# Kernel tuning notes

Measured on AMD Instinct MI355X. Metric: run time of the kernel, lower is better.

Reference implementation:

```python
import jax, jax.numpy as jnp
import numpy as np
from jax import lax

WS = 8
NH = 16

def _conv1x1(t, w):
    # w: (Cout, Cin), t: (B,C,H,W)
    return jnp.einsum('oc,bchw->bohw', w, t)

def _bn(t, g, b, m, v, eps=1e-5):
    s = g * lax.rsqrt(v + eps)
    return (t - m[:, None, None]) * s[:, None, None] + b[:, None, None]

def _forward(x, qkv_w, l2_w, bn2_g, bn2_b, bn2_m, bn2_v, wq, wk, wv, rel_x, rel_y,
             l1_bias, rel_table, dw_w, bnp_g, bnp_b, bnp_m, bnp_v, pw_w):
    B, C, H, W = x.shape
    ws, nh = WS, NH
    d = C // nh
    scale = d ** -0.5

    # ---- local2: 1x1 conv + BN (inference) ----
    local = _bn(_conv1x1(x, l2_w), bn2_g, bn2_b, bn2_m, bn2_v)

    # ---- local1: SelfAttentionConv2d, k=3, pad=1, groups=1 ----
    xp = jnp.pad(x, ((0, 0), (0, 0), (1, 1), (1, 1)))  # zero pad
    vq = _conv1x1(xp, wq)
    vk = _conv1x1(xp, wk)
    vv = _conv1x1(xp, wv)
    win_q = vq[:, :, 1:H + 1, 1:W + 1]  # center crop -> (B,C,H,W)
    def patches3(t):
        p = jnp.stack([t[:, :, i:i + H, j:j + W] for i in range(3) for j in range(3)], axis=-1)
        return p.reshape(B, C, H, W, 3, 3)
    pk = patches3(vk)
    pv = patches3(vv)
    rs = C // 2
    qx = jnp.einsum('bxhw,xk->bhwk', win_q[:, :rs], rel_x)  # (B,H,W,3)
    qy = jnp.einsum('byhw,yk->bhwk', win_q[:, rs:], rel_y)
    logits = jnp.einsum('bchw,bchwkl->bhwkl', win_q, pk)
    logits = logits + qx[:, :, :, None, :] + qy[:, :, :, :, None]
    a = jax.nn.softmax(logits.reshape(B, H, W, 9), axis=-1).reshape(B, H, W, 3, 3)
    local = local + jnp.einsum('bhwkl,bchwkl->bchw', a, pv) + l1_bias[None, :, None, None]

    # ---- windowed MHSA (H, W divisible by ws so pad() is a no-op) ----
    qkv = _conv1x1(x, qkv_w)  # (B, 3C, H, W)
    hh, ww = H // ws, W // ws
    t = qkv.reshape(B, 3, nh, d, hh, ws, ww, ws)
    t = t.transpose(1, 0, 4, 6, 2, 5, 7, 3).reshape(3, B * hh * ww, nh, ws * ws, d)
    q, k, v = t[0], t[1], t[2]
    dots = jnp.einsum('wnid,wnjd->wnij', q, k) * scale
    # relative position bias
    coords = np.stack(np.meshgrid(np.arange(ws), np.arange(ws), indexing='ij')).reshape(2, -1)
    rel = (coords[:, :, None] - coords[:, None, :]).transpose(1, 2, 0) + (ws - 1)
    idx = rel[..., 0] * (2 * ws - 1) + rel[..., 1]  # (ws*ws, ws*ws)
    rpb = rel_table[idx.reshape(-1)].reshape(ws * ws, ws * ws, nh).transpose(2, 0, 1)
    dots = dots + rpb[None]
    attn = jnp.einsum('wnij,wnjd->wnid', jax.nn.softmax(dots, axis=-1), v)
    attn = attn.reshape(B, hh, ww, nh, ws, ws, d).transpose(0, 3, 6, 1, 4, 2, 5).reshape(B, C, H, W)

    # ---- pooling edge-correction branches ----
    pad_h = jnp.pad(attn, ((0, 0), (0, 0), (0, 1), (0, 0)), mode='reflect')
    pad_w = jnp.pad(attn, ((0, 0), (0, 0), (0, 0), (0, 1)), mode='reflect')
    p = ws // 2 - 1
    mph = lax.reduce_window(pad_h, -jnp.inf, lax.max, (1, 1, ws, 1), (1, 1, 1, 1),
                            [(0, 0), (0, 0), (p, p), (0, 0)])
    mpw = lax.reduce_window(pad_w, -jnp.inf, lax.max, (1, 1, 1, ws), (1, 1, 1, 1),
                            [(0, 0), (0, 0), (0, 0), (p, p)])
    aph = lax.reduce_window(pad_h, 0.0, lax.add, (1, 1, ws, 1), (1, 1, 1, 1),
                            [(0, 0), (0, 0), (p, p), (0, 0)]) / ws
    apw = lax.reduce_window(pad_w, 0.0, lax.add, (1, 1, 1, ws), (1, 1, 1, 1),
                            [(0, 0), (0, 0), (0, 0), (p, p)]) / ws
    out = mph + mpw + aph + apw + local

    # ---- proj: reflect pad_out + depthwise 8x8 conv (pad 3) + BN + 1x1 ----
    out = jnp.pad(out, ((0, 0), (0, 0), (0, 1), (0, 1)), mode='reflect')
    out = lax.conv_general_dilated(out, dw_w, (1, 1), [(3, 3), (3, 3)],
                                   dimension_numbers=('NCHW', 'OIHW', 'NCHW'),
                                   feature_group_count=C)
    out = _bn(out, bnp_g, bnp_b, bnp_m, bnp_v)
    out = _conv1x1(out, pw_w)
    return out[:, :, :H, :W]


def setup_inputs() -> dict:
    key = jax.random.key(0)
    ks = jax.random.split(key, 20)
    C = 256
    n = lambda k, shp, s=1.0: jax.random.normal(k, shp, dtype=jnp.float32) * s
    u = lambda k, shp: jax.random.uniform(k, shp, dtype=jnp.float32, minval=0.5, maxval=1.5)
    fan = 1.0 / 16.0  # 1/sqrt(256)
    return {
        'x': n(ks[0], (2, C, 96, 96)),
        'qkv_w': n(ks[1], (3 * C, C), fan),
        'l2_w': n(ks[2], (C, C), fan),
        'bn2_g': u(ks[3], (C,)), 'bn2_b': n(ks[4], (C,), 0.1),
        'bn2_m': n(ks[5], (C,), 0.1), 'bn2_v': u(ks[6], (C,)),
        'wq': n(ks[7], (C, C), fan), 'wk': n(ks[8], (C, C), fan), 'wv': n(ks[9], (C, C), fan),
        'rel_x': n(ks[10], (C // 2, 3), 0.1), 'rel_y': n(ks[11], (C // 2, 3), 0.1),
        'l1_bias': n(ks[12], (C,), 0.05),
        'rel_table': n(ks[13], (15 * 15, NH), 0.02),
        'dw_w': n(ks[14], (C, 1, 8, 8), 1.0 / 8.0),
        'bnp_g': u(ks[15], (C,)), 'bnp_b': n(ks[16], (C,), 0.1),
        'bnp_m': n(ks[17], (C,), 0.1), 'bnp_v': u(ks[18], (C,)),
        'pw_w': n(ks[19], (C, C), fan),
    }


def reference(x, qkv_w, l2_w, bn2_g, bn2_b, bn2_m, bn2_v, wq, wk, wv, rel_x, rel_y,
              l1_bias, rel_table, dw_w, bnp_g, bnp_b, bnp_m, bnp_v, pw_w):
    return _forward(x, qkv_w, l2_w, bn2_g, bn2_b, bn2_m, bn2_v, wq, wk, wv, rel_x, rel_y,
                    l1_bias, rel_table, dw_w, bnp_g, bnp_b, bnp_m, bnp_v, pw_w)
```

## Files before the change

kernel.cpp:

```cpp
#include <hip/hip_runtime.h>
#include <math.h>


namespace {

constexpr int NP = 96 * 96;
constexpr int C  = 256;

typedef __bf16 bf16x8 __attribute__((ext_vector_type(8)));
typedef __bf16 bf16x4 __attribute__((ext_vector_type(4)));
typedef float  f32x4  __attribute__((ext_vector_type(4)));
typedef float  f32x16 __attribute__((ext_vector_type(16)));

__device__ __forceinline__ unsigned short f2bf_rne(float f) {
  unsigned u = __float_as_uint(f);
  u += 0x7FFFu + ((u >> 16) & 1u);
  return (unsigned short)(u >> 16);
}
__device__ __forceinline__ __bf16 f2bf16(float f) {
  unsigned short s = f2bf_rne(f);
  return *(__bf16*)&s;
}
__device__ __forceinline__ float bf2f(unsigned short s) {
  unsigned u = (unsigned)s << 16;
  return __uint_as_float(u);
}
__device__ __forceinline__ float4 bf4_to_f4(const unsigned short* p) {
  bf16x4 v = *(const bf16x4*)p;
  float4 r;
  r.x = (float)v[0]; r.y = (float)v[1]; r.z = (float)v[2]; r.w = (float)v[3];
  return r;
}

__global__ __launch_bounds__(256) void prep(
    const float* __restrict__ x,
    const float* __restrict__ l2, const float* __restrict__ q,
    const float* __restrict__ k,  const float* __restrict__ v,
    const float* __restrict__ qkv, const float* __restrict__ pw,
    unsigned short* __restrict__ XT, unsigned short* __restrict__ W7)
{
  __shared__ float tile[64][65];
  const int bx = blockIdx.x;
  const int t = threadIdx.x;
  if (bx < 2048) {
    const int row = bx;
    const float* src; int r;
    if      (row <  256) { src = l2;  r = row; }
    else if (row <  512) { src = q;   r = row - 256; }
    else if (row <  768) { src = k;   r = row - 512; }
    else if (row < 1024) { src = v;   r = row - 768; }
    else if (row < 1792) { src = qkv; r = row - 1024; }
    else                 { src = pw;  r = row - 1792; }
    W7[row * 256 + t] = f2bf_rne(src[r * 256 + t]);
    return;
  }
  const int xb = bx - 2048;
  const int p0 = (xb % 144) * 64;
  const int c0 = ((xb / 144) % 4) * 64;
  const int b  = xb / 576;
  const float* xb_p = x + (long)b * C * NP;
#pragma unroll
  for (int i = 0; i < 4; ++i) {
    int s = i * 256 + t;
    int c = s >> 4, p4 = s & 15;
    float4 vv = *(const float4*)&xb_p[(long)(c0 + c) * NP + p0 + p4 * 4];
    tile[c][p4 * 4 + 0] = vv.x;
    tile[c][p4 * 4 + 1] = vv.y;
    tile[c][p4 * 4 + 2] = vv.z;
    tile[c][p4 * 4 + 3] = vv.w;
  }
  __syncthreads();
  unsigned short* XTb = XT + (long)b * NP * 256;
#pragma unroll
  for (int i = 0; i < 2; ++i) {
    int s = i * 256 + t;
    int p = s >> 3, c8 = s & 7;
    unsigned short u[8];
#pragma unroll
    for (int e = 0; e < 8; ++e) u[e] = f2bf_rne(tile[c8 * 8 + e][p]);
    *(uint4*)&XTb[(long)(p0 + p) * 256 + c0 + c8 * 8] = *(const uint4*)u;
  }
}

__global__ __launch_bounds__(256) void xpose(
    const float* __restrict__ x, unsigned short* __restrict__ XT)
{
  __shared__ float tile[64][65];
  const int t = threadIdx.x;
  const int p0 = blockIdx.x * 64, c0 = blockIdx.y * 64, b = blockIdx.z;
  const float* xb = x + (long)b * C * NP;
#pragma unroll
  for (int i = 0; i < 4; ++i) {
    int s = i * 256 + t;
    int c = s >> 4, p4 = s & 15;
    float4 v = *(const float4*)&xb[(long)(c0 + c) * NP + p0 + p4 * 4];
    tile[c][p4 * 4 + 0] = v.x;
    tile[c][p4 * 4 + 1] = v.y;
    tile[c][p4 * 4 + 2] = v.z;
    tile[c][p4 * 4 + 3] = v.w;
  }
  __syncthreads();
  unsigned short* XTb = XT + (long)b * NP * 256;
#pragma unroll
  for (int i = 0; i < 2; ++i) {
    int s = i * 256 + t;
    int p = s >> 3, c8 = s & 7;
    unsigned short u[8];
#pragma unroll
    for (int e = 0; e < 8; ++e) u[e] = f2bf_rne(tile[c8 * 8 + e][p]);
    *(uint4*)&XTb[(long)(p0 + p) * 256 + c0 + c8 * 8] = *(const uint4*)u;
  }
}

__global__ __launch_bounds__(256) void gemm_bt(
    const unsigned short* __restrict__ W, const unsigned short* __restrict__ XT,
    unsigned short* __restrict__ O, int Mstride)
{
  __shared__ __align__(16) char smem[36864];
  unsigned short (*As)[40] = reinterpret_cast<unsigned short(*)[40]>(smem);
  unsigned short (*Bs)[40] = reinterpret_cast<unsigned short(*)[40]>(smem + 10240);

  const int t = threadIdx.x;
  const int lane = t & 63, wid = t >> 6;
  const int wm = wid >> 1, wn = wid & 1;
  const int l15 = lane & 15, l4 = lane >> 4;
  const int n0 = blockIdx.x * 128, m0 = blockIdx.y * 128;
  const unsigned short* XTb = XT + (long)blockIdx.z * NP * 256;
  unsigned short* Ob = O + (long)blockIdx.z * NP * Mstride;

  f32x4 acc[4][4];
#pragma unroll
  for (int i = 0; i < 4; ++i)
#pragma unroll
    for (int j = 0; j < 4; ++j) acc[i][j] = (f32x4){0.f, 0.f, 0.f, 0.f};

  for (int k0 = 0; k0 < 256; k0 += 32) {
#pragma unroll
    for (int i = 0; i < 2; ++i) {
      int s = i * 256 + t, r = s >> 2, kc = s & 3;
      *(uint4*)&As[r][kc * 8] =
          *(const uint4*)&W[(long)(m0 + r) * 256 + k0 + kc * 8];
    }
#pragma unroll
    for (int i = 0; i < 2; ++i) {
      int s = i * 256 + t, r = s >> 2, kc = s & 3;
      *(uint4*)&Bs[r][kc * 8] =
          *(const uint4*)&XTb[(long)(n0 + r) * 256 + k0 + kc * 8];
    }
    __syncthreads();

    bf16x8 af[4], bb[4];
#pragma unroll
    for (int mf = 0; mf < 4; ++mf)
      af[mf] = *(const bf16x8*)&As[wm * 64 + mf * 16 + l15][l4 * 8];
#pragma unroll
    for (int nf = 0; nf < 4; ++nf)
      bb[nf] = *(const bf16x8*)&Bs[wn * 64 + nf * 16 + l15][l4 * 8];
#pragma unroll
    for (int mf = 0; mf < 4; ++mf)
#pragma unroll
      for (int nf = 0; nf < 4; ++nf)
        acc[mf][nf] = __builtin_amdgcn_mfma_f32_16x16x32_bf16(
            af[mf], bb[nf], acc[mf][nf], 0, 0, 0);
    __syncthreads();
  }

  unsigned short* trw = (unsigned short*)smem + wid * 64 * 72;
#pragma unroll
  for (int mf = 0; mf < 4; ++mf)
#pragma unroll
    for (int nf = 0; nf < 4; ++nf) {
      unsigned u0 = (unsigned)f2bf_rne(acc[mf][nf][0]) |
                    ((unsigned)f2bf_rne(acc[mf][nf][1]) << 16);
      unsigned u1 = (unsigned)f2bf_rne(acc[mf][nf][2]) |
                    ((unsigned)f2bf_rne(acc[mf][nf][3]) << 16);
      uint2 uu; uu.x = u0; uu.y = u1;
      *(uint2*)&trw[(nf * 16 + l15) * 72 + mf * 16 + l4 * 4] = uu;
    }
  __syncthreads();

  const long pix = n0 + wn * 64 + lane;
  const long rowbase = pix * Mstride + m0 + wm * 64;
#pragma unroll
  for (int cc = 0; cc < 8; ++cc)
    *(uint4*)&Ob[rowbase + cc * 8] = *(const uint4*)&trw[lane * 72 + cc * 8];
}

__global__ __launch_bounds__(256) void gemm_cf32(
    const unsigned short* __restrict__ W, const unsigned short* __restrict__ XT,
    float* __restrict__ Co)
{
  __shared__ unsigned short As[64][40];
  __shared__ unsigned short Bs[128][40];

  const int t = threadIdx.x;
  const int lane = t & 63, wid = t >> 6;
  const int wm = wid >> 1, wn = wid & 1;
  const int l15 = lane & 15, l4 = lane >> 4;
  const int n0 = blockIdx.x * 128, m0 = blockIdx.y * 64;
  const unsigned short* XTb = XT + (long)blockIdx.z * NP * 256;
  float* Cb = Co + (long)blockIdx.z * C * NP;

  f32x4 acc[2][4];
#pragma unroll
  for (int i = 0; i < 2; ++i)
#pragma unroll
    for (int j = 0; j < 4; ++j) acc[i][j] = (f32x4){0.f, 0.f, 0.f, 0.f};

  for (int k0 = 0; k0 < 256; k0 += 32) {
    {
      int r = t >> 2, kc = t & 3;
      *(uint4*)&As[r][kc * 8] =
          *(const uint4*)&W[(long)(m0 + r) * 256 + k0 + kc * 8];
    }
#pragma unroll
    for (int i = 0; i < 2; ++i) {
      int s = i * 256 + t, r = s >> 2, kc = s & 3;
      *(uint4*)&Bs[r][kc * 8] =
          *(const uint4*)&XTb[(long)(n0 + r) * 256 + k0 + kc * 8];
    }
    __syncthreads();

    bf16x8 af[2], bb[4];
#pragma unroll
    for (int mf = 0; mf < 2; ++mf)
      af[mf] = *(const bf16x8*)&As[wm * 32 + mf * 16 + l15][l4 * 8];
#pragma unroll
    for (int nf = 0; nf < 4; ++nf)
      bb[nf] = *(const bf16x8*)&Bs[wn * 64 + nf * 16 + l15][l4 * 8];
#pragma unroll
    for (int mf = 0; mf < 2; ++mf)
#pragma unroll
      for (int nf = 0; nf < 4; ++nf)
        acc[mf][nf] = __builtin_amdgcn_mfma_f32_16x16x32_bf16(
            af[mf], bb[nf], acc[mf][nf], 0, 0, 0);
    __syncthreads();
  }

#pragma unroll
  for (int mf = 0; mf < 2; ++mf)
#pragma unroll
    for (int r = 0; r < 4; ++r) {
      int row = m0 + wm * 32 + mf * 16 + l4 * 4 + r;
#pragma unroll
      for (int nf = 0; nf < 4; ++nf) {
        int col = n0 + wn * 64 + nf * 16 + l15;
        Cb[(long)row * NP + col] = acc[mf][nf][r];
      }
    }
}

__global__ __launch_bounds__(256) void local_attn2(
    const unsigned short* __restrict__ GA,
    const float* __restrict__ rel_x, const float* __restrict__ rel_y,
    const float* __restrict__ bn2_g, const float* __restrict__ bn2_b,
    const float* __restrict__ bn2_m, const float* __restrict__ bn2_v,
    const float* __restrict__ l1_bias, unsigned short* __restrict__ localO)
{
  const int b = blockIdx.y, t = threadIdx.x;
  const int px = t & 31, ch = t >> 5;
  const int p = blockIdx.x * 32 + px;
  const unsigned short* Gb = GA + (long)b * NP * 1024;

  __shared__ float red[8][32][13];
  __shared__ float srel[256 * 3];
  __shared__ float sS[256], sO[256], sBias[256];

  if (t < 128) {
    srel[t * 3 + 0] = rel_x[t * 3 + 0];
    srel[t * 3 + 1] = rel_x[t * 3 + 1];
    srel[t * 3 + 2] = rel_x[t * 3 + 2];
  } else {
    int r = t - 128;
    srel[t * 3 + 0] = rel_y[r * 3 + 0];
    srel[t * 3 + 1] = rel_y[r * 3 + 1];
    srel[t * 3 + 2] = rel_y[r * 3 + 2];
  }
  {
    float s = bn2_g[t] * rsqrtf(bn2_v[t] + 1e-5f);
    sS[t] = s;
    sO[t] = bn2_b[t] - bn2_m[t] * s;
    sBias[t] = l1_bias[t];
  }

  const int h = p / 96, w = p % 96;
  int nof[9];
  float msk[9];
#pragma unroll
  for (int ky = 0; ky < 3; ++ky)
#pragma unroll
    for (int kx = 0; kx < 3; ++kx) {
      int j = ky * 3 + kx, hn = h + ky - 1, wn = w + kx - 1;
      bool v = (hn >= 0 && hn < 96 && wn >= 0 && wn < 96);
      nof[j] = v ? hn * 96 + wn : p;
      msk[j] = v ? 1.f : 0.f;
    }
  __syncthreads();

  float lg[9] = {0, 0, 0, 0, 0, 0, 0, 0, 0};
  float rq[3] = {0, 0, 0};
  const int c0 = ch * 32;
#pragma unroll
  for (int i = 0; i < 4; ++i) {
    const int c = c0 + i * 8;
    bf16x8 q8 = *(const bf16x8*)&Gb[(long)p * 1024 + 256 + c];
    float qv[8];
#pragma unroll
    for (int e = 0; e < 8; ++e) qv[e] = (float)q8[e];
#pragma unroll
    for (int j = 0; j < 9; ++j) {
      bf16x8 k8 = *(const bf16x8*)&Gb[(long)nof[j] * 1024 + 512 + c];
#pragma unroll
      for (int e = 0; e < 8; ++e) lg[j] += qv[e] * (float)k8[e];
    }
#pragma unroll
    for (int e = 0; e < 8; ++e) {
      const float* sr = &srel[(c + e) * 3];
      rq[0] += qv[e] * sr[0];
      rq[1] += qv[e] * sr[1];
      rq[2] += qv[e] * sr[2];
    }
  }
#pragma unroll
  for (int j = 0; j < 9; ++j) red[ch][px][j] = lg[j] * msk[j];
#pragma unroll
  for (int l = 0; l < 3; ++l) red[ch][px][9 + l] = rq[l];
  __syncthreads();

  float a[9];
  float mx = -1e30f;
#pragma unroll
  for (int j = 0; j < 9; ++j) {
    float v = 0.f;
#pragma unroll
    for (int u = 0; u < 8; ++u) v += red[u][px][j];
    float qxl = red[0][px][9 + j % 3] + red[1][px][9 + j % 3] +
                red[2][px][9 + j % 3] + red[3][px][9 + j % 3];
    float qyk = red[4][px][9 + j / 3] + red[5][px][9 + j / 3] +
                red[6][px][9 + j / 3] + red[7][px][9 + j / 3];
    a[j] = v + qxl + qyk;
    mx = fmaxf(mx, a[j]);
  }
  float sum = 0.f;
#pragma unroll
  for (int j = 0; j < 9; ++j) { a[j] = __expf(a[j] - mx); sum += a[j]; }
  const float inv = 1.f / sum;
  float am[9];
#pragma unroll
  for (int j = 0; j < 9; ++j) am[j] = a[j] * inv * msk[j];

#pragma unroll
  for (int i = 0; i < 4; ++i) {
    const int c = c0 + i * 8;
    bf16x8 l28 = *(const bf16x8*)&Gb[(long)p * 1024 + 0 + c];
    float o8[8] = {0, 0, 0, 0, 0, 0, 0, 0};
#pragma unroll
    for (int j = 0; j < 9; ++j) {
      bf16x8 v8 = *(const bf16x8*)&Gb[(long)nof[j] * 1024 + 768 + c];
#pragma unroll
      for (int e = 0; e < 8; ++e) o8[e] += am[j] * (float)v8[e];
    }
#pragma unroll
    for (int e = 0; e < 8; ++e) {
      const int cg = c + e;
      localO[((long)b * C + cg) * NP + p] = f2bf_rne(
          (float)l28[e] * sS[cg] + sO[cg] + o8[e] + sBias[cg]);
    }
  }
}

__global__ __launch_bounds__(64) void window_attn_mfma(
    const unsigned short* __restrict__ QKV,
    const float* __restrict__ rel_table, unsigned short* __restrict__ attnO)
{
  const int win = blockIdx.x, hd = blockIdx.y, b = blockIdx.z;
  const int wy = win / 12, wx = win % 12;
  const int lane = threadIdx.x;
  const int l15 = lane & 15, hi4 = lane >> 4;
  const int l31 = lane & 31, hi2 = lane >> 5;

  __shared__ float srpb[225];
  __shared__ __bf16 P[64][72];

  for (int i = lane; i < 225; i += 64) srpb[i] = rel_table[i * 16 + hd];

  const __bf16* base = (const __bf16*)QKV + (long)b * 9216 * 768;
  const int pixbase = (wy * 8) * 96 + wx * 8;

#define WPIX(i) (pixbase + ((i) >> 3) * 96 + ((i) & 7))

  bf16x8 kf[2], qf[2];
#pragma unroll
  for (int kt = 0; kt < 2; ++kt)
    kf[kt] = *(const bf16x8*)&base[(long)WPIX(32 * kt + l31) * 768 + 256 +
                                   hd * 16 + hi2 * 8];
#pragma unroll
  for (int qt = 0; qt < 2; ++qt)
    qf[qt] = *(const bf16x8*)&base[(long)WPIX(32 * qt + l31) * 768 +
                                   hd * 16 + hi2 * 8];

  bf16x8 vf[2];
#pragma unroll
  for (int kc = 0; kc < 2; ++kc)
#pragma unroll
    for (int j = 0; j < 8; ++j)
      vf[kc][j] = base[(long)WPIX(32 * kc + 8 * hi4 + j) * 768 + 512 +
                       hd * 16 + l15];

  f32x16 S[2][2];
#pragma unroll
  for (int kt = 0; kt < 2; ++kt)
#pragma unroll
    for (int qt = 0; qt < 2; ++qt)
#pragma unroll
      for (int r = 0; r < 16; ++r) S[kt][qt][r] = 0.f;

#pragma unroll
  for (int kt = 0; kt < 2; ++kt)
#pragma unroll
    for (int qt = 0; qt < 2; ++qt)
      S[kt][qt] = __builtin_amdgcn_mfma_f32_32x32x16_bf16(
          kf[kt], qf[qt], S[kt][qt], 0, 0, 0);

  __syncthreads();

  float mx[2] = {-1e30f, -1e30f};
#pragma unroll
  for (int kt = 0; kt < 2; ++kt)
#pragma unroll
    for (int r = 0; r < 16; ++r) {
      const int key = 32 * kt + (r & 3) + 8 * (r >> 2) + 4 * hi2;
      const int ky = key >> 3, kx = key & 7;
#pragma unroll
      for (int qt = 0; qt < 2; ++qt) {
        const int q = 32 * qt + l31;
        const int qy = q >> 3, qx = q & 7;
        float s = S[kt][qt][r] * 0.25f + srpb[(qy - ky + 7) * 15 + (qx - kx + 7)];
        S[kt][qt][r] = s;
        mx[qt] = fmaxf(mx[qt], s);
      }
    }
#pragma unroll
  for (int qt = 0; qt < 2; ++qt)
    mx[qt] = fmaxf(mx[qt], __shfl_xor(mx[qt], 32));

  float sum[2] = {0.f, 0.f};
#pragma unroll
  for (int kt = 0; kt < 2; ++kt)
#pragma unroll
    for (int qt = 0; qt < 2; ++qt)
#pragma unroll
      for (int r = 0; r < 16; ++r) {
        float e = __expf(S[kt][qt][r] - mx[qt]);
        S[kt][qt][r] = e;
        sum[qt] += e;
      }
#pragma unroll
  for (int qt = 0; qt < 2; ++qt) sum[qt] += __shfl_xor(sum[qt], 32);
  const float inv0 = 1.f / sum[0], inv1 = 1.f / sum[1];

#pragma unroll
  for (int qt = 0; qt < 2; ++qt) {
    const float inv = qt ? inv1 : inv0;
#pragma unroll
    for (int kt = 0; kt < 2; ++kt)
#pragma unroll
      for (int rq = 0; rq < 4; ++rq) {
        bf16x4 pk;
#pragma unroll
        for (int j = 0; j < 4; ++j) pk[j] = f2bf16(S[kt][qt][rq * 4 + j] * inv);
        *(bf16x4*)&P[32 * qt + l31][32 * kt + 8 * rq + 4 * hi2] = pk;
      }
  }
  __syncthreads();

  f32x4 o[4];
#pragma unroll
  for (int qt4 = 0; qt4 < 4; ++qt4) o[qt4] = (f32x4){0.f, 0.f, 0.f, 0.f};
#pragma unroll
  for (int kc = 0; kc < 2; ++kc)
#pragma unroll
    for (int qt4 = 0; qt4 < 4; ++qt4) {
      bf16x8 pf = *(const bf16x8*)&P[16 * qt4 + l15][32 * kc + 8 * hi4];
      o[qt4] = __builtin_amdgcn_mfma_f32_16x16x32_bf16(vf[kc], pf, o[qt4], 0, 0, 0);
    }

#pragma unroll
  for (int qt4 = 0; qt4 < 4; ++qt4)
#pragma unroll
    for (int r = 0; r < 4; ++r) {
      const int q = 16 * qt4 + l15;
      attnO[((long)b * C + hd * 16 + 4 * hi4 + r) * NP + WPIX(q)] =
          f2bf_rne(o[qt4][r]);
    }
#undef WPIX
}

__global__ __launch_bounds__(256) void pool_dw7(
    const unsigned short* __restrict__ attn,
    const unsigned short* __restrict__ localO,
    const float* __restrict__ dww,
    const float* __restrict__ bnp_g, const float* __restrict__ bnp_b,
    const float* __restrict__ bnp_m, const float* __restrict__ bnp_v,
    float* __restrict__ dst)
{
  const int bid = blockIdx.x;
  const int r0 = (bid & 3) * 24;
  const int c = bid >> 2;
  const int t = threadIdx.x;

  __shared__ float img[38 * 112];
  __shared__ float img2[31 * 108];

  float wr[64];
#pragma unroll
  for (int i = 0; i < 64; ++i) wr[i] = dww[c * 64 + i];
  const float scl = bnp_g[c] * rsqrtf(bnp_v[c] + 1e-5f);
  const float off = bnp_b[c] - bnp_m[c] * scl;

  for (int b = 0; b < 2; ++b) {
    const unsigned short* A = attn + ((long)b * C + c) * NP;
    const unsigned short* L = localO + ((long)b * C + c) * NP;
    if (b) __syncthreads();

    for (int idx = t; idx < 38 * 28; idx += 256) {
      const int j = idx / 28, k = idx % 28;
      const int R = r0 - 6 + j;
      const bool rv = (R >= 0 && R <= 96);
      const int Rc = (R == 96) ? 94 : (rv ? R : 0);
      const int s0 = 4 * k - 8;
      float4 v = {-1e30f, -1e30f, -1e30f, -1e30f};
      if (rv && s0 >= 0 && s0 <= 92) v = bf4_to_f4(&A[Rc * 96 + s0]);
      else if (rv && s0 == 96) v.x = bf2f(A[Rc * 96 + 94]);
      *(float4*)&img[j * 112 + 4 * k] = v;
    }
    for (int idx = t; idx < 31 * 26; idx += 256) {
      const int j2 = idx / 26, g = idx % 26;
      const int R2 = r0 - 3 + j2;
      const bool rv = (R2 >= 0 && R2 <= 96);
      const int R2c = (R2 == 96) ? 94 : (rv ? R2 : 0);
      float4 v = {0.f, 0.f, 0.f, 0.f};
      if (rv && g >= 1 && g <= 24) v = bf4_to_f4(&L[R2c * 96 + 4 * g - 4]);
      else if (rv && g == 25) v.x = bf2f(L[R2c * 96 + 94]);
      *(float4*)&img2[j2 * 108 + 4 * g] = v;
    }
    __syncthreads();

    for (int idx = t; idx < 31 * 26; idx += 256) {
      const int j2 = idx / 26, g = idx % 26;
      const int R2 = r0 - 3 + j2;
      const bool rv = (R2 >= 0 && R2 <= 96);
      if (!rv || g == 0) continue;
      const int R2c = (R2 == 96) ? 94 : R2;
      const int jb = R2c - r0 + 6;
      float4 out;
      if (g < 25) {
        float mph[4] = {-1e30f, -1e30f, -1e30f, -1e30f};
        float aph[4] = {0.f, 0.f, 0.f, 0.f};
#pragma unroll
        for (int ii = 0; ii < 8; ++ii) {
          float4 hv = *(const float4*)&img[(jb - 3 + ii) * 112 + 4 * g + 4];
          const float h4[4] = {hv.x, hv.y, hv.z, hv.w};
#pragma unroll
          for (int d = 0; d < 4; ++d) {
            mph[d] = fmaxf(mph[d], h4[d]);
            aph[d] += (h4[d] > -1e29f) ? h4[d] : 0.f;
          }
        }
        float r[12];
        {
          float4 a0 = *(const float4*)&img[jb * 112 + 4 * g];
          float4 a1 = *(const float4*)&img[jb * 112 + 4 * g + 4];
          float4 a2 = *(const float4*)&img[jb * 112 + 4 * g + 8];
          r[0] = a0.x; r[1] = a0.y; r[2] = a0.z; r[3] = a0.w;
          r[4] = a1.x; r[5] = a1.y; r[6] = a1.z; r[7] = a1.w;
          r[8] = a2.x; r[9] = a2.y; r[10] = a2.z; r[11] = a2.w;
        }
        float4 lv = *(const float4*)&img2[j2 * 108 + 4 * g];
        const float l4[4] = {lv.x, lv.y, lv.z, lv.w};
        float o4[4];
#pragma unroll
        for (int d = 0; d < 4; ++d) {
          float mpw = -1e30f, apw = 0.f;
#pragma unroll
          for (int ii = 0; ii < 8; ++ii) {
            const float wv = r[d + 1 + ii];
            mpw = fmaxf(mpw, wv);
            apw += (wv > -1e29f) ? wv : 0.f;
          }
          o4[d] = mph[d] + mpw + (aph[d] + apw) * 0.125f + l4[d];
        }
        out.x = o4[0]; out.y = o4[1]; out.z = o4[2]; out.w = o4[3];
      } else {
        float mph = -1e30f, aph = 0.f;
#pragma unroll
        for (int ii = 0; ii < 8; ++ii) {
          const float hv = img[(jb - 3 + ii) * 112 + 102];
          mph = fmaxf(mph, hv);
          aph += (hv > -1e29f) ? hv : 0.f;
        }
        float mpw = -1e30f, apw = 0.f;
#pragma unroll
        for (int ii = 0; ii < 8; ++ii) {
          const float wv = img[jb * 112 + 99 + ii];
          mpw = fmaxf(mpw, wv);
          apw += (wv > -1e29f) ? wv : 0.f;
        }
        out.x = mph + mpw + (aph + apw) * 0.125f + img2[j2 * 108 + 100];
        out.y = 0.f; out.z = 0.f; out.w = 0.f;
      }
      *(float4*)&img2[j2 * 108 + 4 * g] = out;
    }
    __syncthreads();

#pragma unroll
    for (int ss = 0; ss < 2; ++ss) {
      const int seg = ss * 256 + t;
      if (seg >= 288) break;
      const int hh = seg / 12, w0 = (seg % 12) * 8;
      float acc[8] = {0, 0, 0, 0, 0, 0, 0, 0};
#pragma unroll
      for (int i = 0; i < 8; ++i) {
        const float* row = &img2[(hh + i) * 108 + w0];
        float win16[16];
        {
          float4 a0 = *(const float4*)&row[0];
          float4 a1 = *(const float4*)&row[4];
          float4 a2 = *(const float4*)&row[8];
          float4 a3 = *(const float4*)&row[12];
          win16[0] = a0.x;  win16[1] = a0.y;  win16[2] = a0.z;  win16[3] = a0.w;
          win16[4] = a1.x;  win16[5] = a1.y;  win16[6] = a1.z;  win16[7] = a1.w;
          win16[8] = a2.x;  win16[9] = a2.y;  win16[10] = a2.z; win16[11] = a2.w;
          win16[12] = a3.x; win16[13] = a3.y; win16[14] = a3.z; win16[15] = a3.w;
        }
#pragma unroll
        for (int j = 0; j < 8; ++j)
#pragma unroll
          for (int jj = 0; jj < 8; ++jj)
            acc[j] = fmaf(wr[i * 8 + jj], win16[1 + j + jj], acc[j]);
      }
      float4 s0, s1;
      s0.x = acc[0] * scl + off; s0.y = acc[1] * scl + off;
      s0.z = acc[2] * scl + off; s0.w = acc[3] * scl + off;
      s1.x = acc[4] * scl + off; s1.y = acc[5] * scl + off;
      s1.z = acc[6] * scl + off; s1.w = acc[7] * scl + off;
      float* o = dst + ((long)b * C + c) * NP + (r0 + hh) * 96 + w0;
      *(float4*)o = s0;
      *((float4*)o + 1) = s1;
    }
  }
}

}

extern "C" void kernel_launch(void* const* d_in, const int* in_sizes, int n_in,
                              void* d_out, int out_size, void* d_ws, size_t ws_size,
                              hipStream_t stream) {
  const float* x         = (const float*)d_in[0];
  const float* qkv_w     = (const float*)d_in[1];
  const float* l2_w      = (const float*)d_in[2];
  const float* bn2_g     = (const float*)d_in[3];
  const float* bn2_b     = (const float*)d_in[4];
  const float* bn2_m     = (const float*)d_in[5];
  const float* bn2_v     = (const float*)d_in[6];
  const float* wq        = (const float*)d_in[7];
  const float* wk        = (const float*)d_in[8];
  const float* wv        = (const float*)d_in[9];
  const float* rel_x     = (const float*)d_in[10];
  const float* rel_y     = (const float*)d_in[11];
  const float* l1_bias   = (const float*)d_in[12];
  const float* rel_table = (const float*)d_in[13];
  const float* dw_w      = (const float*)d_in[14];
  const float* bnp_g     = (const float*)d_in[15];
  const float* bnp_b     = (const float*)d_in[16];
  const float* bnp_m     = (const float*)d_in[17];
  const float* bnp_v     = (const float*)d_in[18];
  const float* pw_w      = (const float*)d_in[19];
  float* out = (float*)d_out;
  float* ws  = (float*)d_ws;

  unsigned short* GA     = (unsigned short*)ws;
  unsigned short* GB     = (unsigned short*)ws;
  float*          dwB    = ws;
  unsigned short* XT2    = (unsigned short*)(ws + 4718592);
  unsigned short* localB = (unsigned short*)(ws + 9437184);
  unsigned short* attnB  = (unsigned short*)(ws + 14155776);
  unsigned short* W7     = (unsigned short*)(ws + 20971520);
  unsigned short* XT     = (unsigned short*)(ws + 21233664);

  prep<<<dim3(3200), 256, 0, stream>>>(x, l2_w, wq, wk, wv, qkv_w, pw_w,
                                       XT, W7);

  gemm_bt<<<dim3(72, 8, 2), 256, 0, stream>>>(W7, XT, GA, 1024);

  local_attn2<<<dim3(288, 2), 256, 0, stream>>>(GA, rel_x, rel_y, bn2_g, bn2_b,
                                                bn2_m, bn2_v, l1_bias, localB);

  gemm_bt<<<dim3(72, 6, 2), 256, 0, stream>>>(W7 + 1024 * 256, XT, GB, 768);

  window_attn_mfma<<<dim3(144, 16, 2), 64, 0, stream>>>(GB, rel_table, attnB);

  pool_dw7<<<dim3(1024), 256, 0, stream>>>(attnB, localB, dw_w, bnp_g,
                                           bnp_b, bnp_m, bnp_v, dwB);

  xpose<<<dim3(144, 4, 2), 256, 0, stream>>>(dwB, XT2);

  gemm_cf32<<<dim3(72, 4, 2), 256, 0, stream>>>(W7 + 1792 * 256, XT2, out);
}
```

Baseline: 178.8 us.

## Retile pool+depthwise kernel into 12-row tiles with register row reuse

The pooling plus depthwise-conv kernel now uses one block per (12-row tile, channel, batch) with 128 threads, replacing blocks that looped over both batches with 24-row tiles. Pool threads compute 4 consecutive output rows from 11 cached register rows, and conv threads compute 4x4 outputs from 11 shared rows, which cuts redundant LDS reads. The goal is more parallel blocks and less shared-memory traffic. In exchange, halo overhead per tile goes up, and only 72 of 128 threads do the conv phase, while edge-row replication is handled by special cases.

```diff
diff --git a/kernel.cpp b/kernel.cpp
--- a/kernel.cpp
+++ b/kernel.cpp
@@ -496,7 +496,7 @@
 #undef WPIX
 }
 
-__global__ __launch_bounds__(256) void pool_dw7(
+__global__ __launch_bounds__(128) void pool_dw8(
     const unsigned short* __restrict__ attn,
     const unsigned short* __restrict__ localO,
     const float* __restrict__ dww,
@@ -504,79 +504,87 @@
     const float* __restrict__ bnp_m, const float* __restrict__ bnp_v,
     float* __restrict__ dst)
 {
-  const int bid = blockIdx.x;
-  const int r0 = (bid & 3) * 24;
-  const int c = bid >> 2;
+  const int r0 = blockIdx.x * 12;
+  const int c = blockIdx.y, b = blockIdx.z;
   const int t = threadIdx.x;
 
-  __shared__ float img[38 * 112];
-  __shared__ float img2[31 * 108];
-
+  __shared__ float img[26 * 116];
+  __shared__ float img2[19 * 108];
+
+  const unsigned short* A = attn + ((long)b * C + c) * NP;
+  const unsigned short* L = localO + ((long)b * C + c) * NP;
+
+  for (int idx = t; idx < 26 * 28; idx += 128) {
+    const int j = idx / 28, k = idx % 28;
+    const int R = r0 - 6 + j;
+    const bool rv = (R >= 0 && R <= 96);
+    const int Rc = (R == 96) ? 94 : (rv ? R : 0);
+    const int s0 = 4 * k - 8;
+    float4 v = {-1e30f, -1e30f, -1e30f, -1e30f};
+    if (rv && s0 >= 0 && s0 <= 92) v = bf4_to_f4(&A[Rc * 96 + s0]);
+    else if (rv && s0 == 96) v.x = bf2f(A[Rc * 96 + 94]);
+    *(float4*)&img[j * 116 + 4 * k] = v;
+  }
+  for (int idx = t; idx < 19 * 27; idx += 128) {
+    const int j2 = idx / 27, g = idx % 27;
+    const int R2 = r0 - 3 + j2;
+    const bool rv = (R2 >= 0 && R2 <= 96);
+    const int R2c = (R2 == 96) ? 94 : (rv ? R2 : 0);
+    const int w0 = 4 * g - 4;
+    float4 v = {0.f, 0.f, 0.f, 0.f};
+    if (rv) {
+      if (w0 >= 0 && w0 <= 92) v = bf4_to_f4(&L[R2c * 96 + w0]);
+      else if (w0 == 96) v.x = bf2f(L[R2c * 96 + 94]);
+    }
+    *(float4*)&img2[j2 * 108 + 4 * g] = v;
+  }
   float wr[64];
 #pragma unroll
   for (int i = 0; i < 64; ++i) wr[i] = dww[c * 64 + i];
   const float scl = bnp_g[c] * rsqrtf(bnp_v[c] + 1e-5f);
   const float off = bnp_b[c] - bnp_m[c] * scl;
-
-  for (int b = 0; b < 2; ++b) {
-    const unsigned short* A = attn + ((long)b * C + c) * NP;
-    const unsigned short* L = localO + ((long)b * C + c) * NP;
-    if (b) __syncthreads();
-
-    for (int idx = t; idx < 38 * 28; idx += 256) {
-      const int j = idx / 28, k = idx % 28;
-      const int R = r0 - 6 + j;
-      const bool rv = (R >= 0 && R <= 96);
-      const int Rc = (R == 96) ? 94 : (rv ? R : 0);
-      const int s0 = 4 * k - 8;
-      float4 v = {-1e30f, -1e30f, -1e30f, -1e30f};
-      if (rv && s0 >= 0 && s0 <= 92) v = bf4_to_f4(&A[Rc * 96 + s0]);
-      else if (rv && s0 == 96) v.x = bf2f(A[Rc * 96 + 94]);
-      *(float4*)&img[j * 112 + 4 * k] = v;
-    }
-    for (int idx = t; idx < 31 * 26; idx += 256) {
-      const int j2 = idx / 26, g = idx % 26;
-      const int R2 = r0 - 3 + j2;
-      const bool rv = (R2 >= 0 && R2 <= 96);
-      const int R2c = (R2 == 96) ? 94 : (rv ? R2 : 0);
-      float4 v = {0.f, 0.f, 0.f, 0.f};
-      if (rv && g >= 1 && g <= 24) v = bf4_to_f4(&L[R2c * 96 + 4 * g - 4]);
-      else if (rv && g == 25) v.x = bf2f(L[R2c * 96 + 94]);
-      *(float4*)&img2[j2 * 108 + 4 * g] = v;
-    }
-    __syncthreads();
-
-    for (int idx = t; idx < 31 * 26; idx += 256) {
-      const int j2 = idx / 26, g = idx % 26;
-      const int R2 = r0 - 3 + j2;
-      const bool rv = (R2 >= 0 && R2 <= 96);
-      if (!rv || g == 0) continue;
-      const int R2c = (R2 == 96) ? 94 : R2;
-      const int jb = R2c - r0 + 6;
-      float4 out;
-      if (g < 25) {
+  __syncthreads();
+
+  const int j2lo = (r0 == 0) ? 3 : 0;
+  const int j2hi = (r0 == 84) ? 14 : 18;
+  if (t < 120) {
+    const int blk = t / 24, G = t % 24;
+    const int j2b = j2lo + blk * 4;
+    if (j2b <= j2hi) {
+      float4 hc[11];
+#pragma unroll
+      for (int ii = 0; ii < 11; ++ii) {
+        int rr = j2b + ii;
+        rr = (rr > 25) ? 25 : rr;
+        hc[ii] = *(const float4*)&img[rr * 116 + 4 * G + 8];
+      }
+#pragma unroll
+      for (int r = 0; r < 4; ++r) {
+        const int j2 = j2b + r;
+        if (j2 > j2hi) break;
         float mph[4] = {-1e30f, -1e30f, -1e30f, -1e30f};
         float aph[4] = {0.f, 0.f, 0.f, 0.f};
 #pragma unroll
         for (int ii = 0; ii < 8; ++ii) {
-          float4 hv = *(const float4*)&img[(jb - 3 + ii) * 112 + 4 * g + 4];
-          const float h4[4] = {hv.x, hv.y, hv.z, hv.w};
+          const float h4[4] = {hc[r + ii].x, hc[r + ii].y, hc[r + ii].z,
+                               hc[r + ii].w};
 #pragma unroll
           for (int d = 0; d < 4; ++d) {
             mph[d] = fmaxf(mph[d], h4[d]);
             aph[d] += (h4[d] > -1e29f) ? h4[d] : 0.f;
           }
         }
-        float r[12];
+        float rw[12];
         {
-          float4 a0 = *(const float4*)&img[jb * 112 + 4 * g];
-          float4 a1 = *(const float4*)&img[jb * 112 + 4 * g + 4];
-          float4 a2 = *(const float4*)&img[jb * 112 + 4 * g + 8];
-          r[0] = a0.x; r[1] = a0.y; r[2] = a0.z; r[3] = a0.w;
-          r[4] = a1.x; r[5] = a1.y; r[6] = a1.z; r[7] = a1.w;
-          r[8] = a2.x; r[9] = a2.y; r[10] = a2.z; r[11] = a2.w;
+          const float* row = &img[(j2 + 3) * 116 + 4 * G + 4];
+          float4 a0 = *(const float4*)&row[0];
+          float4 a1 = *(const float4*)&row[4];
+          float4 a2 = *(const float4*)&row[8];
+          rw[0] = a0.x; rw[1] = a0.y; rw[2] = a0.z; rw[3] = a0.w;
+          rw[4] = a1.x; rw[5] = a1.y; rw[6] = a1.z; rw[7] = a1.w;
+          rw[8] = a2.x; rw[9] = a2.y; rw[10] = a2.z; rw[11] = a2.w;
         }
-        float4 lv = *(const float4*)&img2[j2 * 108 + 4 * g];
+        float4 lv = *(const float4*)&img2[j2 * 108 + 4 * G + 4];
         const float l4[4] = {lv.x, lv.y, lv.z, lv.w};
         float o4[4];
 #pragma unroll
@@ -584,69 +592,64 @@
           float mpw = -1e30f, apw = 0.f;
 #pragma unroll
           for (int ii = 0; ii < 8; ++ii) {
-            const float wv = r[d + 1 + ii];
+            const float wv = rw[d + 1 + ii];
             mpw = fmaxf(mpw, wv);
             apw += (wv > -1e29f) ? wv : 0.f;
           }
           o4[d] = mph[d] + mpw + (aph[d] + apw) * 0.125f + l4[d];
         }
+        float4 out;
         out.x = o4[0]; out.y = o4[1]; out.z = o4[2]; out.w = o4[3];
-      } else {
-        float mph = -1e30f, aph = 0.f;
-#pragma unroll
-        for (int ii = 0; ii < 8; ++ii) {
-          const float hv = img[(jb - 3 + ii) * 112 + 102];
-          mph = fmaxf(mph, hv);
-          aph += (hv > -1e29f) ? hv : 0.f;
+        *(float4*)&img2[j2 * 108 + 4 * G + 4] = out;
+        if (G == 23) img2[j2 * 108 + 100] = o4[2];
+        if (r0 == 84 && j2 == 13) {
+          *(float4*)&img2[15 * 108 + 4 * G + 4] = out;
+          if (G == 23) img2[15 * 108 + 100] = o4[2];
         }
-        float mpw = -1e30f, apw = 0.f;
-#pragma unroll
-        for (int ii = 0; ii < 8; ++ii) {
-          const float wv = img[jb * 112 + 99 + ii];
-          mpw = fmaxf(mpw, wv);
-          apw += (wv > -1e29f) ? wv : 0.f;
-        }
-        out.x = mph + mpw + (aph + apw) * 0.125f + img2[j2 * 108 + 100];
-        out.y = 0.f; out.z = 0.f; out.w = 0.f;
       }
-      *(float4*)&img2[j2 * 108 + 4 * g] = out;
-    }
-    __syncthreads();
-
-#pragma unroll
-    for (int ss = 0; ss < 2; ++ss) {
-      const int seg = ss * 256 + t;
-      if (seg >= 288) break;
-      const int hh = seg / 12, w0 = (seg % 12) * 8;
-      float acc[8] = {0, 0, 0, 0, 0, 0, 0, 0};
-#pragma unroll
-      for (int i = 0; i < 8; ++i) {
-        const float* row = &img2[(hh + i) * 108 + w0];
-        float win16[16];
-        {
-          float4 a0 = *(const float4*)&row[0];
-          float4 a1 = *(const float4*)&row[4];
-          float4 a2 = *(const float4*)&row[8];
-          float4 a3 = *(const float4*)&row[12];
-          win16[0] = a0.x;  win16[1] = a0.y;  win16[2] = a0.z;  win16[3] = a0.w;
-          win16[4] = a1.x;  win16[5] = a1.y;  win16[6] = a1.z;  win16[7] = a1.w;
-          win16[8] = a2.x;  win16[9] = a2.y;  win16[10] = a2.z; win16[11] = a2.w;
-          win16[12] = a3.x; win16[13] = a3.y; win16[14] = a3.z; win16[15] = a3.w;
-        }
-#pragma unroll
-        for (int j = 0; j < 8; ++j)
+    }
+  }
+  __syncthreads();
+
+  if (t < 72) {
+    const int cb = t / 24, ocg = t % 24;
+    const int hh0 = cb * 4;
+    float acc[4][4];
+#pragma unroll
+    for (int o = 0; o < 4; ++o)
+#pragma unroll
+      for (int d = 0; d < 4; ++d) acc[o][d] = 0.f;
+#pragma unroll
+    for (int i = 0; i < 11; ++i) {
+      const float* row = &img2[(hh0 + i) * 108 + 4 * ocg];
+      float w12[12];
+      {
+        float4 a0 = *(const float4*)&row[0];
+        float4 a1 = *(const float4*)&row[4];
+        float4 a2 = *(const float4*)&row[8];
+        w12[0] = a0.x; w12[1] = a0.y; w12[2] = a0.z; w12[3] = a0.w;
+        w12[4] = a1.x; w12[5] = a1.y; w12[6] = a1.z; w12[7] = a1.w;
+        w12[8] = a2.x; w12[9] = a2.y; w12[10] = a2.z; w12[11] = a2.w;
+      }
+#pragma unroll
+      for (int o = 0; o < 4; ++o) {
+        if (o > i || i - o > 7) continue;
+        const int ir = i - o;
+#pragma unroll
+        for (int d = 0; d < 4; ++d)
 #pragma unroll
           for (int jj = 0; jj < 8; ++jj)
-            acc[j] = fmaf(wr[i * 8 + jj], win16[1 + j + jj], acc[j]);
+            acc[o][d] = fmaf(wr[ir * 8 + jj], w12[d + 1 + jj], acc[o][d]);
       }
-      float4 s0, s1;
-      s0.x = acc[0] * scl + off; s0.y = acc[1] * scl + off;
-      s0.z = acc[2] * scl + off; s0.w = acc[3] * scl + off;
-      s1.x = acc[4] * scl + off; s1.y = acc[5] * scl + off;
-      s1.z = acc[6] * scl + off; s1.w = acc[7] * scl + off;
-      float* o = dst + ((long)b * C + c) * NP + (r0 + hh) * 96 + w0;
-      *(float4*)o = s0;
-      *((float4*)o + 1) = s1;
+    }
+#pragma unroll
+    for (int o = 0; o < 4; ++o) {
+      float4 s;
+      s.x = acc[o][0] * scl + off;
+      s.y = acc[o][1] * scl + off;
+      s.z = acc[o][2] * scl + off;
+      s.w = acc[o][3] * scl + off;
+      *(float4*)&dst[((long)b * C + c) * NP + (r0 + hh0 + o) * 96 + 4 * ocg] = s;
     }
   }
 }
@@ -700,8 +703,8 @@
 
   window_attn_mfma<<<dim3(144, 16, 2), 64, 0, stream>>>(GB, rel_table, attnB);
 
-  pool_dw7<<<dim3(1024), 256, 0, stream>>>(attnB, localB, dw_w, bnp_g,
-                                           bnp_b, bnp_m, bnp_v, dwB);
+  pool_dw8<<<dim3(8, 256, 2), 128, 0, stream>>>(attnB, localB, dw_w, bnp_g,
+                                                bnp_b, bnp_m, bnp_v, dwB);
 
   xpose<<<dim3(144, 4, 2), 256, 0, stream>>>(dwB, XT2);
 
```

Measured after the change: 175.8 us. No clear change (-1.6%).
